# Kernel tuning notes

Measured on AMD Instinct MI355X. Metric: run time of the kernel, lower is better.

Reference implementation:

```python
import jax, jax.numpy as jnp
import numpy as np

MU_DT = 0.01
INIT_STD = 0.05

# hidden layers use tanh; last layer is identity (utils.Linear())

def setup_inputs() -> dict:
    key = jax.random.key(0)
    ks = jax.random.split(key, 7)
    B = 512
    nodes = [1024, 4096, 4096, 3072]
    img_batch = jax.random.normal(ks[0], (B, nodes[3]), dtype=jnp.float32)
    mu0 = INIT_STD * jax.random.normal(ks[1], (B, nodes[0]), dtype=jnp.float32)
    mu1 = INIT_STD * jax.random.normal(ks[2], (B, nodes[1]), dtype=jnp.float32)
    mu2 = INIT_STD * jax.random.normal(ks[3], (B, nodes[2]), dtype=jnp.float32)
    W0 = jax.random.normal(ks[4], (nodes[0], nodes[1]), dtype=jnp.float32) / jnp.sqrt(jnp.float32(nodes[0]))
    W1 = jax.random.normal(ks[5], (nodes[1], nodes[2]), dtype=jnp.float32) / jnp.sqrt(jnp.float32(nodes[1]))
    W2 = jax.random.normal(ks[6], (nodes[2], nodes[3]), dtype=jnp.float32) / jnp.sqrt(jnp.float32(nodes[2]))
    return {"img_batch": img_batch, "mu0": mu0, "mu1": mu1, "mu2": mu2,
            "W0": W0, "W1": W1, "W2": W2, "n_iters": 20}


def reference(img_batch, mu0, mu1, mu2, W0, W1, W2, n_iters):
    Ws = (W0, W1, W2)
    L = 3  # n_layers
    acts = (jnp.tanh, jnp.tanh, lambda h: h)
    dacts = (lambda h: 1.0 - jnp.tanh(h) ** 2,
             lambda h: 1.0 - jnp.tanh(h) ** 2,
             lambda h: jnp.ones_like(h))

    def preds_errs(mus):
        # preds[0] = 0, so errs[0] = mus[0]
        hs, errs = [], [mus[0]]
        for l in range(L):
            h = mus[l] @ Ws[l]          # [B, nodes[l+1]]
            hs.append(h)
            errs.append(mus[l + 1] - acts[l](h))
        return hs, errs

    def body(mus, _):
        # prediction pass with current mus (matches stored layer inputs/errs)
        hs, errs = preds_errs(mus)
        new_mus = []
        for l in range(L):
            back = (errs[l + 1] * dacts[l](hs[l])) @ Ws[l].T
            new_mus.append(mus[l] + MU_DT * (back - errs[l]))
        new_mus.append(mus[L])  # target clamped
        return tuple(new_mus), None

    mus = (mu0, mu1, mu2, img_batch)
    mus, _ = jax.lax.scan(body, mus, None, length=n_iters)
    # final prediction/error pass (end of last torch iteration)
    _, errs = preds_errs(mus)
    return jnp.concatenate(errs, axis=1)  # [B, 1024+4096+4096+3072]
```

## Files before the change

kernel.cpp:

```cpp
#include <hip/hip_runtime.h>
#include <hip/hip_bf16.h>
#include <stdint.h>

typedef __hip_bfloat16 bf16_t;
typedef __attribute__((ext_vector_type(8))) short bf16x8;
typedef __attribute__((ext_vector_type(4))) float f32x4;

#define MU_DT 0.01f

__device__ inline void gload_lds16(const void* g, void* lds) {
  __builtin_amdgcn_global_load_lds((const __attribute__((address_space(1))) void*)g,
                                   (__attribute__((address_space(3))) void*)lds, 16, 0, 0);
}

struct GemmLayer {
  const bf16_t* A;
  const bf16_t* Bt;
  const float*  X;
  const float*  E;
  float*        O1;
  bf16_t*       O2;
  int K, N, ostride, mode;
};

struct Seg { int start, layer, tmBase, tilesN; };

struct GemmArgs {
  GemmLayer L[3];
  Seg seg[8];
};

__global__ __launch_bounds__(512) void gemm_merged(GemmArgs args) {
  __shared__ __align__(16) bf16_t As[2 * 64 * 64];
  __shared__ __align__(16) bf16_t Bs[2 * 128 * 64];

  const int bid = blockIdx.x;
  int s = 0;
#pragma unroll
  for (int i = 1; i < 8; ++i)
    if (bid >= args.seg[i].start) s = i;
  const Seg sg = args.seg[s];
  const GemmLayer Lr = args.L[sg.layer];
  const int local = bid - sg.start;
  const int tm = sg.tmBase + local / sg.tilesN;
  const int tn = local % sg.tilesN;
  const int K = Lr.K;
  const int rowBase = tm * 64;
  const int colBase = tn * 128;

  const int tid  = threadIdx.x;
  const int lane = tid & 63;
  const int wv   = tid >> 6;
  const int wrM  = wv >> 2;
  const int wcN  = wv & 3;
  const int lo   = lane & 15, hi = lane >> 4;

  f32x4 acc[2][2];
#pragma unroll
  for (int m = 0; m < 2; ++m)
#pragma unroll
    for (int n = 0; n < 2; ++n)
      acc[m][n] = f32x4{0.f, 0.f, 0.f, 0.f};

  char* AsB = (char*)As;
  char* BsB = (char*)Bs;

  const bf16_t* pA0;
  const bf16_t* pB[2];
  {
    const int c = tid;
    const int r = c >> 3, sw = (c & 7) ^ (r & 7);
    pA0 = Lr.A + (size_t)(rowBase + r) * K + sw * 8;
  }
#pragma unroll
  for (int j = 0; j < 2; ++j) {
    const int c = j * 512 + tid;
    const int r = c >> 3, sw = (c & 7) ^ (r & 7);
    pB[j] = Lr.Bt + (size_t)(colBase + r) * K + sw * 8;
  }

  int aoff[2][2], boff[2][2];
#pragma unroll
  for (int m = 0; m < 2; ++m) {
    const int row = wrM * 32 + m * 16 + lo;
#pragma unroll
    for (int kk = 0; kk < 2; ++kk)
      aoff[m][kk] = row * 128 + (((kk * 4 + hi) ^ (row & 7)) << 4);
  }
#pragma unroll
  for (int n = 0; n < 2; ++n) {
    const int row = wcN * 32 + n * 16 + lo;
#pragma unroll
    for (int kk = 0; kk < 2; ++kk)
      boff[n][kk] = row * 128 + (((kk * 4 + hi) ^ (row & 7)) << 4);
  }

  const int waveB = wv * 1024;
  const int nkt = K >> 6;

  gload_lds16(pA0,   AsB + waveB);
  gload_lds16(pB[0], BsB + waveB);
  gload_lds16(pB[1], BsB + 8192 + waveB);
  __syncthreads();

  int cur = 0;
  for (int kt = 0; kt < nkt; ++kt) {
    const int curA = cur * 8192, curB = cur * 16384;
    if (kt + 1 < nkt) {
      const int ke = (kt + 1) * 64;
      gload_lds16(pA0 + ke,   AsB + (curA ^ 8192) + waveB);
      gload_lds16(pB[0] + ke, BsB + (curB ^ 16384) + waveB);
      gload_lds16(pB[1] + ke, BsB + (curB ^ 16384) + 8192 + waveB);
    }

    bf16x8 a[2][2], b[2][2];
#pragma unroll
    for (int m = 0; m < 2; ++m)
#pragma unroll
      for (int kk = 0; kk < 2; ++kk)
        a[m][kk] = *(const bf16x8*)(AsB + curA + aoff[m][kk]);
#pragma unroll
    for (int n = 0; n < 2; ++n)
#pragma unroll
      for (int kk = 0; kk < 2; ++kk)
        b[n][kk] = *(const bf16x8*)(BsB + curB + boff[n][kk]);

#pragma unroll
    for (int kk = 0; kk < 2; ++kk)
#pragma unroll
      for (int m = 0; m < 2; ++m)
#pragma unroll
        for (int n = 0; n < 2; ++n)
          acc[m][n] = __builtin_amdgcn_mfma_f32_16x16x32_bf16(a[m][kk], b[n][kk], acc[m][n], 0, 0, 0);

    if (kt + 1 < nkt) {
      __syncthreads();
      cur ^= 1;
    }
  }

  const int N = Lr.N;
#pragma unroll
  for (int m = 0; m < 2; ++m) {
#pragma unroll
    for (int n = 0; n < 2; ++n) {
#pragma unroll
      for (int r = 0; r < 4; ++r) {
        const int row = rowBase + wrM * 32 + m * 16 + hi * 4 + r;
        const int col = colBase + wcN * 32 + n * 16 + lo;
        const float v = acc[m][n][r];
        const size_t iN = (size_t)row * N + col;
        const size_t iO = (size_t)row * Lr.ostride + col;
        if (Lr.mode == 0) {
          const float mu = Lr.X[iN];
          const float t  = tanhf(v);
          const float e  = mu - t;
          Lr.O1[iO] = e;
          Lr.O2[iN] = __float2bfloat16(e * (1.0f - t * t));
        } else if (Lr.mode == 1) {
          const float e = Lr.X[iN] - v;
          Lr.O1[iO] = e;
          Lr.O2[iN] = __float2bfloat16(e);
        } else if (Lr.mode == 2) {
          const float mu = Lr.X[iN];
          const float nv = mu + MU_DT * (v - mu);
          Lr.O1[iN] = nv;
          Lr.O2[iN] = __float2bfloat16(nv);
        } else {
          const float mu = Lr.X[iN];
          const float e  = Lr.E[iN];
          const float nv = mu + MU_DT * (v - e);
          Lr.O1[iN] = nv;
          Lr.O2[iN] = __float2bfloat16(nv);
        }
      }
    }
  }
}

__global__ void prep_weight(const float* __restrict__ W, bf16_t* __restrict__ Wb,
                            bf16_t* __restrict__ WTb, int R, int C) {
  __shared__ bf16_t t[64][65];
  const int tx = threadIdx.x, ty = threadIdx.y;
  const int c0 = blockIdx.x * 64, r0 = blockIdx.y * 64;
  for (int rr = ty; rr < 64; rr += 4) {
    const float v = W[(size_t)(r0 + rr) * C + c0 + tx];
    const bf16_t b = __float2bfloat16(v);
    Wb[(size_t)(r0 + rr) * C + c0 + tx] = b;
    t[rr][tx] = b;
  }
  __syncthreads();
  for (int rr = ty; rr < 64; rr += 4) {
    WTb[(size_t)(c0 + rr) * R + r0 + tx] = t[tx][rr];
  }
}

__global__ void copy_cast(const float* __restrict__ in, float* __restrict__ of,
                          bf16_t* __restrict__ ob, int n) {
  const int i = blockIdx.x * blockDim.x + threadIdx.x;
  if (i < n) {
    const float v = in[i];
    of[i] = v;
    ob[i] = __float2bfloat16(v);
  }
}

__global__ void copy_e0(const float* __restrict__ mu0, float* __restrict__ out) {
  const int i = blockIdx.x * blockDim.x + threadIdx.x;
  if (i < 512 * 1024) {
    const int b = i >> 10, j = i & 1023;
    out[(size_t)b * 12288 + j] = mu0[i];
  }
}

extern "C" void kernel_launch(void* const* d_in, const int* in_sizes, int n_in,
                              void* d_out, int out_size, void* d_ws, size_t ws_size,
                              hipStream_t stream) {
  const float* img  = (const float*)d_in[0];
  const float* mu0i = (const float*)d_in[1];
  const float* mu1i = (const float*)d_in[2];
  const float* mu2i = (const float*)d_in[3];
  const float* W0   = (const float*)d_in[4];
  const float* W1   = (const float*)d_in[5];
  const float* W2   = (const float*)d_in[6];
  float* out = (float*)d_out;
  const int n_iters = 20;

  char* p = (char*)d_ws;
  auto alloc = [&](size_t bytes) -> char* {
    char* r = p;
    p += (bytes + 255) & ~(size_t)255;
    return r;
  };
  bf16_t* Wb0 = (bf16_t*)alloc((size_t)1024 * 4096 * 2);
  bf16_t* Wb1 = (bf16_t*)alloc((size_t)4096 * 4096 * 2);
  bf16_t* Wb2 = (bf16_t*)alloc((size_t)4096 * 3072 * 2);
  bf16_t* WT0 = (bf16_t*)alloc((size_t)4096 * 1024 * 2);
  bf16_t* WT1 = (bf16_t*)alloc((size_t)4096 * 4096 * 2);
  bf16_t* WT2 = (bf16_t*)alloc((size_t)3072 * 4096 * 2);
  float*  mu0 = (float*)alloc((size_t)512 * 1024 * 4);
  float*  mu1 = (float*)alloc((size_t)512 * 4096 * 4);
  float*  mu2 = (float*)alloc((size_t)512 * 4096 * 4);
  bf16_t* mb0 = (bf16_t*)alloc((size_t)512 * 1024 * 2);
  bf16_t* mb1 = (bf16_t*)alloc((size_t)512 * 4096 * 2);
  bf16_t* mb2 = (bf16_t*)alloc((size_t)512 * 4096 * 2);
  float*  e1  = (float*)alloc((size_t)512 * 4096 * 4);
  float*  e2  = (float*)alloc((size_t)512 * 4096 * 4);
  float*  e3  = (float*)alloc((size_t)512 * 3072 * 4);
  bf16_t* G0  = (bf16_t*)alloc((size_t)512 * 4096 * 2);
  bf16_t* G1  = (bf16_t*)alloc((size_t)512 * 4096 * 2);
  bf16_t* G2  = (bf16_t*)alloc((size_t)512 * 3072 * 2);
  (void)ws_size;

  dim3 tb(64, 4);
  prep_weight<<<dim3(4096 / 64, 1024 / 64), tb, 0, stream>>>(W0, Wb0, WT0, 1024, 4096);
  prep_weight<<<dim3(4096 / 64, 4096 / 64), tb, 0, stream>>>(W1, Wb1, WT1, 4096, 4096);
  prep_weight<<<dim3(3072 / 64, 4096 / 64), tb, 0, stream>>>(W2, Wb2, WT2, 4096, 3072);
  copy_cast<<<(512 * 1024 + 255) / 256, 256, 0, stream>>>(mu0i, mu0, mb0, 512 * 1024);
  copy_cast<<<(512 * 4096 + 255) / 256, 256, 0, stream>>>(mu1i, mu1, mb1, 512 * 4096);
  copy_cast<<<(512 * 4096 + 255) / 256, 256, 0, stream>>>(mu2i, mu2, mb2, 512 * 4096);

  const Seg SENT = { 1 << 30, 0, 0, 1 };

  GemmArgs fa;
  fa.L[0] = { mb0, WT0, mu1, nullptr, e1, G0, 1024, 4096, 4096, 0 };
  fa.L[1] = { mb1, WT1, mu2, nullptr, e2, G1, 4096, 4096, 4096, 0 };
  fa.L[2] = { mb2, WT2, img, nullptr, e3, G2, 4096, 3072, 3072, 1 };
  fa.seg[0] = { 0,   0, 0, 32 };
  fa.seg[1] = { 256, 1, 0, 32 };
  fa.seg[2] = { 512, 2, 0, 24 };
  fa.seg[3] = SENT; fa.seg[4] = SENT; fa.seg[5] = SENT;
  fa.seg[6] = SENT; fa.seg[7] = SENT;
  const int fwdBlocks = 704;

  GemmArgs faF = fa;
  faF.L[0].O1 = out + 1024; faF.L[0].ostride = 12288;
  faF.L[1].O1 = out + 5120; faF.L[1].ostride = 12288;
  faF.L[2].O1 = out + 9216; faF.L[2].ostride = 12288;

  GemmArgs ba;
  ba.L[0] = { G0, Wb0, mu0, nullptr, mu0, mb0, 4096, 1024, 1024, 2 };
  ba.L[1] = { G1, Wb1, mu1, e1,      mu1, mb1, 4096, 4096, 4096, 3 };
  ba.L[2] = { G2, Wb2, mu2, e2,      mu2, mb2, 3072, 4096, 4096, 3 };
  ba.seg[0] = { 0,   2, 0, 32 };
  ba.seg[1] = { 64,  1, 0, 32 };
  ba.seg[2] = { 192, 2, 6, 32 };
  ba.seg[3] = { 256, 2, 2, 32 };
  ba.seg[4] = { 320, 1, 4, 32 };
  ba.seg[5] = { 448, 0, 0, 8 };
  ba.seg[6] = { 512, 2, 4, 32 };
  ba.seg[7] = SENT;
  const int bwdBlocks = 576;

  for (int it = 0; it < n_iters; ++it) {
    gemm_merged<<<fwdBlocks, 512, 0, stream>>>(fa);
    gemm_merged<<<bwdBlocks, 512, 0, stream>>>(ba);
  }
  gemm_merged<<<fwdBlocks, 512, 0, stream>>>(faF);
  copy_e0<<<(512 * 1024 + 255) / 256, 256, 0, stream>>>(mu0, out);
}
```

Measured before the change: 2.502 ms.

## Run iterative forward/backward GEMMs in FP8 with fixed scaling, keep final pass bf16

Adds an FP8 e4m3 GEMM kernel that uses the 16x16x32 fp8 MFMA with K-tile 128. All 20 inner iterations run in FP8, and operands are prescaled by 8 so products are rescaled by 1/64. The last forward pass that writes the output still uses bf16 operands, so the epilogue keeps both fp8 and bf16 copies of the updated mus. The aim is to halve operand bandwidth and double MFMA throughput, at the cost of much coarser precision in the iterative updates, which could break tolerance.

After: 2.222 ms. -11.2%, faster.

```diff
diff --git a/kernel.cpp b/kernel.cpp
--- a/kernel.cpp
+++ b/kernel.cpp
@@ -1,5 +1,6 @@
 #include <hip/hip_runtime.h>
 #include <hip/hip_bf16.h>
+#include <hip/hip_fp8.h>
 #include <stdint.h>
 
 typedef __hip_bfloat16 bf16_t;
@@ -7,10 +8,174 @@
 typedef __attribute__((ext_vector_type(4))) float f32x4;
 
 #define MU_DT 0.01f
+#define S8 8.0f
+#define INV_S64 (1.0f / 64.0f)
+
+__device__ inline uint8_t f2fp8(float x) {
+  __hip_fp8_e4m3 t(x);
+  return t.__x;
+}
 
 __device__ inline void gload_lds16(const void* g, void* lds) {
   __builtin_amdgcn_global_load_lds((const __attribute__((address_space(1))) void*)g,
                                    (__attribute__((address_space(3))) void*)lds, 16, 0, 0);
+}
+
+struct Seg { int start, layer, tmBase, tilesN; };
+
+struct GemmLayer8 {
+  const uint8_t* A;
+  const uint8_t* Bt;
+  const float*  X;
+  const float*  E;
+  float*        O1;
+  uint8_t*      O2a;
+  bf16_t*       O2b;
+  int K, N, mode;
+};
+struct GemmArgs8 { GemmLayer8 L[3]; Seg seg[8]; };
+
+__global__ __launch_bounds__(512) void gemm_fp8(GemmArgs8 args) {
+  __shared__ __align__(16) uint8_t As[2 * 64 * 128];
+  __shared__ __align__(16) uint8_t Bs[2 * 128 * 128];
+
+  const int bid = blockIdx.x;
+  int s = 0;
+#pragma unroll
+  for (int i = 1; i < 8; ++i)
+    if (bid >= args.seg[i].start) s = i;
+  const Seg sg = args.seg[s];
+  const GemmLayer8 Lr = args.L[sg.layer];
+  const int local = bid - sg.start;
+  const int tm = sg.tmBase + local / sg.tilesN;
+  const int tn = local % sg.tilesN;
+  const int K = Lr.K;
+  const int rowBase = tm * 64;
+  const int colBase = tn * 128;
+
+  const int tid  = threadIdx.x;
+  const int lane = tid & 63;
+  const int wv   = tid >> 6;
+  const int wrM  = wv >> 2;
+  const int wcN  = wv & 3;
+  const int lo   = lane & 15, hi = lane >> 4;
+
+  f32x4 acc[2][2];
+#pragma unroll
+  for (int m = 0; m < 2; ++m)
+#pragma unroll
+    for (int n = 0; n < 2; ++n)
+      acc[m][n] = f32x4{0.f, 0.f, 0.f, 0.f};
+
+  char* AsB = (char*)As;
+  char* BsB = (char*)Bs;
+
+  const uint8_t* pA0;
+  const uint8_t* pB[2];
+  {
+    const int c = tid;
+    const int r = c >> 3, sw = (c & 7) ^ (r & 7);
+    pA0 = Lr.A + (size_t)(rowBase + r) * K + sw * 16;
+  }
+#pragma unroll
+  for (int j = 0; j < 2; ++j) {
+    const int c = j * 512 + tid;
+    const int r = c >> 3, sw = (c & 7) ^ (r & 7);
+    pB[j] = Lr.Bt + (size_t)(colBase + r) * K + sw * 16;
+  }
+
+  int aoff[2][4], boff[2][4];
+#pragma unroll
+  for (int m = 0; m < 2; ++m) {
+    const int row = wrM * 32 + m * 16 + lo;
+#pragma unroll
+    for (int kk = 0; kk < 4; ++kk)
+      aoff[m][kk] = row * 128 + (((kk * 2 + (hi >> 1)) ^ (row & 7)) << 4) + ((hi & 1) << 3);
+  }
+#pragma unroll
+  for (int n = 0; n < 2; ++n) {
+    const int row = wcN * 32 + n * 16 + lo;
+#pragma unroll
+    for (int kk = 0; kk < 4; ++kk)
+      boff[n][kk] = row * 128 + (((kk * 2 + (hi >> 1)) ^ (row & 7)) << 4) + ((hi & 1) << 3);
+  }
+
+  const int waveB = wv * 1024;
+  const int nkt = K >> 7;
+
+  gload_lds16(pA0,   AsB + waveB);
+  gload_lds16(pB[0], BsB + waveB);
+  gload_lds16(pB[1], BsB + 8192 + waveB);
+  __syncthreads();
+
+  int cur = 0;
+  for (int kt = 0; kt < nkt; ++kt) {
+    const int curA = cur * 8192, curB = cur * 16384;
+    if (kt + 1 < nkt) {
+      const int ke = (kt + 1) * 128;
+      gload_lds16(pA0 + ke,   AsB + (curA ^ 8192) + waveB);
+      gload_lds16(pB[0] + ke, BsB + (curB ^ 16384) + waveB);
+      gload_lds16(pB[1] + ke, BsB + (curB ^ 16384) + 8192 + waveB);
+    }
+
+    long a[2][4], b[2][4];
+#pragma unroll
+    for (int m = 0; m < 2; ++m)
+#pragma unroll
+      for (int kk = 0; kk < 4; ++kk)
+        a[m][kk] = *(const long*)(AsB + curA + aoff[m][kk]);
+#pragma unroll
+    for (int n = 0; n < 2; ++n)
+#pragma unroll
+      for (int kk = 0; kk < 4; ++kk)
+        b[n][kk] = *(const long*)(BsB + curB + boff[n][kk]);
+
+#pragma unroll
+    for (int kk = 0; kk < 4; ++kk)
+#pragma unroll
+      for (int m = 0; m < 2; ++m)
+#pragma unroll
+        for (int n = 0; n < 2; ++n)
+          acc[m][n] = __builtin_amdgcn_mfma_f32_16x16x32_fp8_fp8(a[m][kk], b[n][kk], acc[m][n], 0, 0, 0);
+
+    if (kt + 1 < nkt) {
+      __syncthreads();
+      cur ^= 1;
+    }
+  }
+
+  const int N = Lr.N;
+#pragma unroll
+  for (int m = 0; m < 2; ++m) {
+#pragma unroll
+    for (int n = 0; n < 2; ++n) {
+#pragma unroll
+      for (int r = 0; r < 4; ++r) {
+        const int row = rowBase + wrM * 32 + m * 16 + hi * 4 + r;
+        const int col = colBase + wcN * 32 + n * 16 + lo;
+        const float v = acc[m][n][r] * INV_S64;
+        const size_t iN = (size_t)row * N + col;
+        if (Lr.mode == 0) {
+          const float mu = Lr.X[iN];
+          const float t  = tanhf(v);
+          const float e  = mu - t;
+          Lr.O1[iN]  = e;
+          Lr.O2a[iN] = f2fp8(e * (1.0f - t * t) * S8);
+        } else if (Lr.mode == 1) {
+          const float e = Lr.X[iN] - v;
+          Lr.O1[iN]  = e;
+          Lr.O2a[iN] = f2fp8(e * S8);
+        } else {
+          const float mu = Lr.X[iN];
+          const float sub = (Lr.mode == 2) ? mu : Lr.E[iN];
+          const float nv = mu + MU_DT * (v - sub);
+          Lr.O1[iN]  = nv;
+          Lr.O2a[iN] = f2fp8(nv * S8);
+          Lr.O2b[iN] = __float2bfloat16(nv);
+        }
+      }
+    }
+  }
 }
 
 struct GemmLayer {
@@ -22,15 +187,9 @@
   bf16_t*       O2;
   int K, N, ostride, mode;
 };
-
-struct Seg { int start, layer, tmBase, tilesN; };
-
-struct GemmArgs {
-  GemmLayer L[3];
-  Seg seg[8];
-};
-
-__global__ __launch_bounds__(512) void gemm_merged(GemmArgs args) {
+struct GemmArgs { GemmLayer L[3]; Seg seg[8]; };
+
+__global__ __launch_bounds__(512) void gemm_bf16(GemmArgs args) {
   __shared__ __align__(16) bf16_t As[2 * 64 * 64];
   __shared__ __align__(16) bf16_t Bs[2 * 128 * 64];
 
@@ -161,46 +320,38 @@
           const float e = Lr.X[iN] - v;
           Lr.O1[iO] = e;
           Lr.O2[iN] = __float2bfloat16(e);
-        } else if (Lr.mode == 2) {
-          const float mu = Lr.X[iN];
-          const float nv = mu + MU_DT * (v - mu);
-          Lr.O1[iN] = nv;
-          Lr.O2[iN] = __float2bfloat16(nv);
-        } else {
-          const float mu = Lr.X[iN];
-          const float e  = Lr.E[iN];
-          const float nv = mu + MU_DT * (v - e);
-          Lr.O1[iN] = nv;
-          Lr.O2[iN] = __float2bfloat16(nv);
         }
       }
     }
   }
 }
 
-__global__ void prep_weight(const float* __restrict__ W, bf16_t* __restrict__ Wb,
-                            bf16_t* __restrict__ WTb, int R, int C) {
-  __shared__ bf16_t t[64][65];
+__global__ void prep_all(const float* __restrict__ W, bf16_t* __restrict__ WTb,
+                         uint8_t* __restrict__ W8, uint8_t* __restrict__ WT8,
+                         int R, int C) {
+  __shared__ float t[64][65];
   const int tx = threadIdx.x, ty = threadIdx.y;
   const int c0 = blockIdx.x * 64, r0 = blockIdx.y * 64;
   for (int rr = ty; rr < 64; rr += 4) {
     const float v = W[(size_t)(r0 + rr) * C + c0 + tx];
-    const bf16_t b = __float2bfloat16(v);
-    Wb[(size_t)(r0 + rr) * C + c0 + tx] = b;
-    t[rr][tx] = b;
+    W8[(size_t)(r0 + rr) * C + c0 + tx] = f2fp8(v * S8);
+    t[rr][tx] = v;
   }
   __syncthreads();
   for (int rr = ty; rr < 64; rr += 4) {
-    WTb[(size_t)(c0 + rr) * R + r0 + tx] = t[tx][rr];
-  }
-}
-
-__global__ void copy_cast(const float* __restrict__ in, float* __restrict__ of,
-                          bf16_t* __restrict__ ob, int n) {
+    const float v = t[tx][rr];
+    WTb[(size_t)(c0 + rr) * R + r0 + tx] = __float2bfloat16(v);
+    WT8[(size_t)(c0 + rr) * R + r0 + tx] = f2fp8(v * S8);
+  }
+}
+
+__global__ void copy_cast3(const float* __restrict__ in, float* __restrict__ of,
+                           uint8_t* __restrict__ o8, bf16_t* __restrict__ ob, int n) {
   const int i = blockIdx.x * blockDim.x + threadIdx.x;
   if (i < n) {
     const float v = in[i];
     of[i] = v;
+    o8[i] = f2fp8(v * S8);
     ob[i] = __float2bfloat16(v);
   }
 }
@@ -232,40 +383,49 @@
     p += (bytes + 255) & ~(size_t)255;
     return r;
   };
-  bf16_t* Wb0 = (bf16_t*)alloc((size_t)1024 * 4096 * 2);
-  bf16_t* Wb1 = (bf16_t*)alloc((size_t)4096 * 4096 * 2);
-  bf16_t* Wb2 = (bf16_t*)alloc((size_t)4096 * 3072 * 2);
   bf16_t* WT0 = (bf16_t*)alloc((size_t)4096 * 1024 * 2);
   bf16_t* WT1 = (bf16_t*)alloc((size_t)4096 * 4096 * 2);
   bf16_t* WT2 = (bf16_t*)alloc((size_t)3072 * 4096 * 2);
-  float*  mu0 = (float*)alloc((size_t)512 * 1024 * 4);
-  float*  mu1 = (float*)alloc((size_t)512 * 4096 * 4);
-  float*  mu2 = (float*)alloc((size_t)512 * 4096 * 4);
-  bf16_t* mb0 = (bf16_t*)alloc((size_t)512 * 1024 * 2);
-  bf16_t* mb1 = (bf16_t*)alloc((size_t)512 * 4096 * 2);
-  bf16_t* mb2 = (bf16_t*)alloc((size_t)512 * 4096 * 2);
-  float*  e1  = (float*)alloc((size_t)512 * 4096 * 4);
-  float*  e2  = (float*)alloc((size_t)512 * 4096 * 4);
-  float*  e3  = (float*)alloc((size_t)512 * 3072 * 4);
-  bf16_t* G0  = (bf16_t*)alloc((size_t)512 * 4096 * 2);
-  bf16_t* G1  = (bf16_t*)alloc((size_t)512 * 4096 * 2);
-  bf16_t* G2  = (bf16_t*)alloc((size_t)512 * 3072 * 2);
+  uint8_t* W80  = (uint8_t*)alloc((size_t)1024 * 4096);
+  uint8_t* W81  = (uint8_t*)alloc((size_t)4096 * 4096);
+  uint8_t* W82  = (uint8_t*)alloc((size_t)4096 * 3072);
+  uint8_t* WT80 = (uint8_t*)alloc((size_t)4096 * 1024);
+  uint8_t* WT81 = (uint8_t*)alloc((size_t)4096 * 4096);
+  uint8_t* WT82 = (uint8_t*)alloc((size_t)3072 * 4096);
+  float*   mu0 = (float*)alloc((size_t)512 * 1024 * 4);
+  float*   mu1 = (float*)alloc((size_t)512 * 4096 * 4);
+  float*   mu2 = (float*)alloc((size_t)512 * 4096 * 4);
+  uint8_t* m80 = (uint8_t*)alloc((size_t)512 * 1024);
+  uint8_t* m81 = (uint8_t*)alloc((size_t)512 * 4096);
+  uint8_t* m82 = (uint8_t*)alloc((size_t)512 * 4096);
+  bf16_t*  mb0 = (bf16_t*)alloc((size_t)512 * 1024 * 2);
+  bf16_t*  mb1 = (bf16_t*)alloc((size_t)512 * 4096 * 2);
+  bf16_t*  mb2 = (bf16_t*)alloc((size_t)512 * 4096 * 2);
+  float*   e1  = (float*)alloc((size_t)512 * 4096 * 4);
+  float*   e2  = (float*)alloc((size_t)512 * 4096 * 4);
+  float*   e3  = (float*)alloc((size_t)512 * 3072 * 4);
+  uint8_t* G80 = (uint8_t*)alloc((size_t)512 * 4096);
+  uint8_t* G81 = (uint8_t*)alloc((size_t)512 * 4096);
+  uint8_t* G82 = (uint8_t*)alloc((size_t)512 * 3072);
+  bf16_t*  Gb0 = (bf16_t*)alloc((size_t)512 * 4096 * 2);
+  bf16_t*  Gb1 = (bf16_t*)alloc((size_t)512 * 4096 * 2);
+  bf16_t*  Gb2 = (bf16_t*)alloc((size_t)512 * 3072 * 2);
   (void)ws_size;
 
   dim3 tb(64, 4);
-  prep_weight<<<dim3(4096 / 64, 1024 / 64), tb, 0, stream>>>(W0, Wb0, WT0, 1024, 4096);
-  prep_weight<<<dim3(4096 / 64, 4096 / 64), tb, 0, stream>>>(W1, Wb1, WT1, 4096, 4096);
-  prep_weight<<<dim3(3072 / 64, 4096 / 64), tb, 0, stream>>>(W2, Wb2, WT2, 4096, 3072);
-  copy_cast<<<(512 * 1024 + 255) / 256, 256, 0, stream>>>(mu0i, mu0, mb0, 512 * 1024);
-  copy_cast<<<(512 * 4096 + 255) / 256, 256, 0, stream>>>(mu1i, mu1, mb1, 512 * 4096);
-  copy_cast<<<(512 * 4096 + 255) / 256, 256, 0, stream>>>(mu2i, mu2, mb2, 512 * 4096);
+  prep_all<<<dim3(4096 / 64, 1024 / 64), tb, 0, stream>>>(W0, WT0, W80, WT80, 1024, 4096);
+  prep_all<<<dim3(4096 / 64, 4096 / 64), tb, 0, stream>>>(W1, WT1, W81, WT81, 4096, 4096);
+  prep_all<<<dim3(3072 / 64, 4096 / 64), tb, 0, stream>>>(W2, WT2, W82, WT82, 4096, 3072);
+  copy_cast3<<<(512 * 1024 + 255) / 256, 256, 0, stream>>>(mu0i, mu0, m80, mb0, 512 * 1024);
+  copy_cast3<<<(512 * 4096 + 255) / 256, 256, 0, stream>>>(mu1i, mu1, m81, mb1, 512 * 4096);
+  copy_cast3<<<(512 * 4096 + 255) / 256, 256, 0, stream>>>(mu2i, mu2, m82, mb2, 512 * 4096);
 
   const Seg SENT = { 1 << 30, 0, 0, 1 };
 
-  GemmArgs fa;
-  fa.L[0] = { mb0, WT0, mu1, nullptr, e1, G0, 1024, 4096, 4096, 0 };
-  fa.L[1] = { mb1, WT1, mu2, nullptr, e2, G1, 4096, 4096, 4096, 0 };
-  fa.L[2] = { mb2, WT2, img, nullptr, e3, G2, 4096, 3072, 3072, 1 };
+  GemmArgs8 fa;
+  fa.L[0] = { m80, WT80, mu1, nullptr, e1, G80, nullptr, 1024, 4096, 0 };
+  fa.L[1] = { m81, WT81, mu2, nullptr, e2, G81, nullptr, 4096, 4096, 0 };
+  fa.L[2] = { m82, WT82, img, nullptr, e3, G82, nullptr, 4096, 3072, 1 };
   fa.seg[0] = { 0,   0, 0, 32 };
   fa.seg[1] = { 256, 1, 0, 32 };
   fa.seg[2] = { 512, 2, 0, 24 };
@@ -273,15 +433,10 @@
   fa.seg[6] = SENT; fa.seg[7] = SENT;
   const int fwdBlocks = 704;
 
-  GemmArgs faF = fa;
-  faF.L[0].O1 = out + 1024; faF.L[0].ostride = 12288;
-  faF.L[1].O1 = out + 5120; faF.L[1].ostride = 12288;
-  faF.L[2].O1 = out + 9216; faF.L[2].ostride = 12288;
-
-  GemmArgs ba;
-  ba.L[0] = { G0, Wb0, mu0, nullptr, mu0, mb0, 4096, 1024, 1024, 2 };
-  ba.L[1] = { G1, Wb1, mu1, e1,      mu1, mb1, 4096, 4096, 4096, 3 };
-  ba.L[2] = { G2, Wb2, mu2, e2,      mu2, mb2, 3072, 4096, 4096, 3 };
+  GemmArgs8 ba;
+  ba.L[0] = { G80, W80, mu0, nullptr, mu0, m80, mb0, 4096, 1024, 2 };
+  ba.L[1] = { G81, W81, mu1, e1,      mu1, m81, mb1, 4096, 4096, 3 };
+  ba.L[2] = { G82, W82, mu2, e2,      mu2, m82, mb2, 3072, 4096, 3 };
   ba.seg[0] = { 0,   2, 0, 32 };
   ba.seg[1] = { 64,  1, 0, 32 };
   ba.seg[2] = { 192, 2, 6, 32 };
@@ -292,10 +447,20 @@
   ba.seg[7] = SENT;
   const int bwdBlocks = 576;
 
+  GemmArgs faF;
+  faF.L[0] = { mb0, WT0, mu1, nullptr, out + 1024, Gb0, 1024, 4096, 12288, 0 };
+  faF.L[1] = { mb1, WT1, mu2, nullptr, out + 5120, Gb1, 4096, 4096, 12288, 0 };
+  faF.L[2] = { mb2, WT2, img, nullptr, out + 9216, Gb2, 4096, 3072, 12288, 1 };
+  faF.seg[0] = { 0,   0, 0, 32 };
+  faF.seg[1] = { 256, 1, 0, 32 };
+  faF.seg[2] = { 512, 2, 0, 24 };
+  faF.seg[3] = SENT; faF.seg[4] = SENT; faF.seg[5] = SENT;
+  faF.seg[6] = SENT; faF.seg[7] = SENT;
+
   for (int it = 0; it < n_iters; ++it) {
-    gemm_merged<<<fwdBlocks, 512, 0, stream>>>(fa);
-    gemm_merged<<<bwdBlocks, 512, 0, stream>>>(ba);
-  }
-  gemm_merged<<<fwdBlocks, 512, 0, stream>>>(faF);
+    gemm_fp8<<<fwdBlocks, 512, 0, stream>>>(fa);
+    gemm_fp8<<<bwdBlocks, 512, 0, stream>>>(ba);
+  }
+  gemm_bf16<<<fwdBlocks, 512, 0, stream>>>(faF);
   copy_e0<<<(512 * 1024 + 255) / 256, 256, 0, stream>>>(mu0, out);
 }
```
